# Kernel tuning notes

Hardware: AMD Instinct MI355X
Metric: run time of the kernel (lower is better)

## Reference

```python
import jax, jax.numpy as jnp
import numpy as np

TOKENS, DIM, DIM_OUT, R, ALPHA = 8192, 4096, 4096, 16, 32
SCALE = ALPHA / R  # 2.0


def setup_inputs() -> dict:
    key = jax.random.key(0)
    k1, k2, k3, k4, k5 = jax.random.split(key, 5)
    x = jax.random.normal(k1, (TOKENS, DIM), dtype=jnp.float32)
    A = jax.random.normal(k2, (DIM, R), dtype=jnp.float32)
    B = jax.random.normal(k3, (R, DIM_OUT), dtype=jnp.float32) * 0.02
    W = jax.random.normal(k4, (DIM_OUT, DIM), dtype=jnp.float32) * 0.02  # base Linear weight
    b = jax.random.normal(k5, (DIM_OUT,), dtype=jnp.float32)
    return {"x": x, "A": A, "B": B, "W": W, "b": b}


def reference(x, A, B, W, b):
    # LoRA path: x @ (A @ B) * scale, computed in the efficient low-rank order
    # (mathematically identical to materializing the full-rank weight).
    lora = ((x @ A) @ B) * SCALE              # [tokens, dim_out]
    base = x @ W.T + b                         # wrapped base Linear forward
    return lora + base
```

## Files before the change

kernel.cpp:

```cpp
#include <hip/hip_runtime.h>
#include <hip/hip_bf16.h>
#include <stdint.h>

#define TOKENS   8192
#define DIM      4096
#define DIM_OUT  4096
#define LORA_R   16
#define LORA_SCALE 2.0f

typedef __bf16 bf16_t;
typedef __attribute__((ext_vector_type(8))) __bf16 bfrag;
typedef __attribute__((ext_vector_type(4))) float f32x4;

__device__ __forceinline__ void gload_lds16(const bf16_t* gsrc, bf16_t* ldst) {
    __builtin_amdgcn_global_load_lds(
        (const __attribute__((address_space(1))) uint32_t*)(const void*)gsrc,
        (__attribute__((address_space(3))) uint32_t*)(void*)ldst,
        16, 0, 0);
}

__global__ void cast_x_kernel(const float* __restrict__ x, bf16_t* __restrict__ xb) {
    const int total = TOKENS * DIM / 8;
    for (int i = blockIdx.x * blockDim.x + threadIdx.x; i < total;
         i += gridDim.x * blockDim.x) {
        const float4* p = reinterpret_cast<const float4*>(x + (size_t)i * 8);
        float4 v0 = p[0], v1 = p[1];
        union { bf16_t o[8]; uint4 u; } pk;
        pk.o[0] = (bf16_t)v0.x; pk.o[1] = (bf16_t)v0.y;
        pk.o[2] = (bf16_t)v0.z; pk.o[3] = (bf16_t)v0.w;
        pk.o[4] = (bf16_t)v1.x; pk.o[5] = (bf16_t)v1.y;
        pk.o[6] = (bf16_t)v1.z; pk.o[7] = (bf16_t)v1.w;
        *reinterpret_cast<uint4*>(xb + (size_t)i * 8) = pk.u;
    }
}

__global__ void weff_kernel(const float* __restrict__ W, const float* __restrict__ A,
                            const float* __restrict__ B, bf16_t* __restrict__ Wt) {
    int idx = blockIdx.x * blockDim.x + threadIdx.x;
    int k0 = (idx & 511) << 3;
    int n0 = (idx >> 9) << 2;

    float bn[4][16];
#pragma unroll
    for (int r = 0; r < 16; ++r) {
        float4 bv = *reinterpret_cast<const float4*>(B + (size_t)r * DIM_OUT + n0);
        bn[0][r] = bv.x; bn[1][r] = bv.y; bn[2][r] = bv.z; bn[3][r] = bv.w;
    }
    float ab[4][8];
#pragma unroll
    for (int j = 0; j < 8; ++j) {
        const float4* ap = reinterpret_cast<const float4*>(A + (size_t)(k0 + j) * LORA_R);
        float4 a0 = ap[0], a1 = ap[1], a2 = ap[2], a3 = ap[3];
        float av[16] = {a0.x,a0.y,a0.z,a0.w,a1.x,a1.y,a1.z,a1.w,
                        a2.x,a2.y,a2.z,a2.w,a3.x,a3.y,a3.z,a3.w};
#pragma unroll
        for (int n = 0; n < 4; ++n) {
            float s = 0.f;
#pragma unroll
            for (int r = 0; r < 16; ++r) s += av[r] * bn[n][r];
            ab[n][j] = s;
        }
    }
#pragma unroll
    for (int n = 0; n < 4; ++n) {
        const float4* wp = reinterpret_cast<const float4*>(W + (size_t)(n0 + n) * DIM + k0);
        float4 w0 = wp[0], w1 = wp[1];
        float wv[8] = {w0.x,w0.y,w0.z,w0.w,w1.x,w1.y,w1.z,w1.w};
        union { bf16_t o[8]; uint4 u; } pk;
#pragma unroll
        for (int j = 0; j < 8; ++j) pk.o[j] = (bf16_t)(wv[j] + LORA_SCALE * ab[n][j]);
        *reinterpret_cast<uint4*>(Wt + (size_t)(n0 + n) * DIM + k0) = pk.u;
    }
}

#define BM 256
#define BN 256
#define BK 64
#define MB_BLKS (TOKENS / BM)
#define NB_BLKS (DIM_OUT / BN)
#define NT      (DIM / BK)

#define BAR() do { __builtin_amdgcn_s_barrier(); __builtin_amdgcn_sched_barrier(0); } while (0)
#define SB0() __builtin_amdgcn_sched_barrier(0)
#define VMWAIT_(n) asm volatile("s_waitcnt vmcnt(" #n ")" ::: "memory")
#define VMWAIT(n) VMWAIT_(n)

__global__ __launch_bounds__(512, 2) void gemm_kernel(
    const bf16_t* __restrict__ Xb, const bf16_t* __restrict__ Wt,
    const float* __restrict__ bias, float* __restrict__ C)
{
    __shared__ __align__(16) bf16_t sA[2][BM][BK];
    __shared__ __align__(16) bf16_t sB[2][BN][BK];

    const int nwg = MB_BLKS * NB_BLKS;
    int bid = blockIdx.x;
    int swz = (bid & 7) * (nwg >> 3) + (bid >> 3);
    int bm = swz / NB_BLKS;
    int bn = swz % NB_BLKS;

    const int tid  = threadIdx.x;
    const int lane = tid & 63;
    const int wid  = tid >> 6;
    const int wr   = wid >> 2;
    const int wc   = wid & 3;

    const int srow = tid >> 3;
    const int scol = (tid & 7) * 8;
    const int koff = (((tid & 7) ^ ((tid >> 3) & 7)) * 8);
    const bf16_t* Ag = Xb + (size_t)(bm * BM + srow) * DIM + koff;
    const bf16_t* Bg = Wt + (size_t)(bn * BN + srow) * DIM + koff;

#define STAGE_A(d, kt) do { \
    const bf16_t* s_ = Ag + (size_t)(kt) * BK; \
    bf16_t* d_ = &sA[d][srow][scol]; \
    gload_lds16(s_,                     d_); \
    gload_lds16(s_ + (size_t)64  * DIM, d_ + 64  * BK); \
    gload_lds16(s_ + (size_t)128 * DIM, d_ + 128 * BK); \
    gload_lds16(s_ + (size_t)192 * DIM, d_ + 192 * BK); \
} while (0)

#define STAGE_B(d, kt) do { \
    const bf16_t* s_ = Bg + (size_t)(kt) * BK; \
    bf16_t* d_ = &sB[d][srow][scol]; \
    gload_lds16(s_,                     d_); \
    gload_lds16(s_ + (size_t)64  * DIM, d_ + 64  * BK); \
    gload_lds16(s_ + (size_t)128 * DIM, d_ + 128 * BK); \
    gload_lds16(s_ + (size_t)192 * DIM, d_ + 192 * BK); \
} while (0)

    const int q     = lane & 7;
    const int kslot = lane >> 4;
    const int r15   = lane & 15;
    const int cK0   = ((kslot    ) ^ q) * 8;
    const int cK1   = ((kslot + 4) ^ q) * 8;
    const int arow0 = wr * 128 + r15;
    const int brow0 = wc * 64  + r15;

    f32x4 acc[8][4] = {};
    bfrag aLo[4][2], aHi[4][2], bLo[2][2], bHi[2][2];

#define READ_A4(dst, dd, mb) do { \
    _Pragma("unroll") \
    for (int m_ = 0; m_ < 4; ++m_) { \
        dst[m_][0] = *reinterpret_cast<const bfrag*>(&sA[dd][arow0 + (mb + m_) * 16][cK0]); \
        dst[m_][1] = *reinterpret_cast<const bfrag*>(&sA[dd][arow0 + (mb + m_) * 16][cK1]); \
    } \
} while (0)

#define READ_B2(dst, dd, nb) do { \
    _Pragma("unroll") \
    for (int n_ = 0; n_ < 2; ++n_) { \
        dst[n_][0] = *reinterpret_cast<const bfrag*>(&sB[dd][brow0 + (nb + n_) * 16][cK0]); \
        dst[n_][1] = *reinterpret_cast<const bfrag*>(&sB[dd][brow0 + (nb + n_) * 16][cK1]); \
    } \
} while (0)

#define MFMA_Q(Af, Bf, mb, nb) do { \
    __builtin_amdgcn_s_setprio(1); \
    _Pragma("unroll") \
    for (int m_ = 0; m_ < 4; ++m_) \
    _Pragma("unroll") \
    for (int n_ = 0; n_ < 2; ++n_) \
    _Pragma("unroll") \
    for (int ks_ = 0; ks_ < 2; ++ks_) \
        acc[mb + m_][nb + n_] = __builtin_amdgcn_mfma_f32_16x16x32_bf16( \
            Af[m_][ks_], Bf[n_][ks_], acc[mb + m_][nb + n_], 0, 0, 0); \
    __builtin_amdgcn_s_setprio(0); \
} while (0)

#define TILE(d, ktn, DO_STAGE, DO_NEXT, VM) do { \
     READ_B2(bHi, d, 2); \
             SB0(); MFMA_Q(aLo, bLo, 0, 0); BAR(); \
     READ_A4(aHi, d, 4); if (DO_STAGE) STAGE_B(d, ktn); \
             SB0(); MFMA_Q(aLo, bHi, 0, 2); VMWAIT(VM); BAR(); \
     if (DO_NEXT) READ_A4(aLo, (d) ^ 1, 0); if (DO_STAGE) STAGE_A(d, ktn); \
             SB0(); MFMA_Q(aHi, bHi, 4, 2); BAR(); \
     MFMA_Q(aHi, bLo, 4, 0); \
             if (DO_NEXT) READ_B2(bLo, (d) ^ 1, 0); BAR(); \
} while (0)

    STAGE_A(0, 0); STAGE_B(0, 0);
    STAGE_B(1, 1); STAGE_A(1, 1);
    VMWAIT(8);
    BAR();
    READ_A4(aLo, 0, 0); READ_B2(bLo, 0, 0);

    for (int it = 0; it < NT / 2 - 1; ++it) {
        int kt0 = 2 * it;
        TILE(0, kt0 + 2, true, true, 4);
        TILE(1, kt0 + 3, true, true, 4);
    }
    TILE(0, 0, false, true, 0);
    TILE(1, 0, false, false, 0);

    int row0 = bm * BM + wr * 128 + (lane >> 4) * 4;
    int col0 = bn * BN + wc * 64 + r15;
#pragma unroll
    for (int n = 0; n < 4; ++n) {
        int c = col0 + n * 16;
        float bv = bias[c];
#pragma unroll
        for (int m = 0; m < 8; ++m) {
            int r = row0 + m * 16;
#pragma unroll
            for (int j = 0; j < 4; ++j)
                C[(size_t)(r + j) * DIM_OUT + c] = acc[m][n][j] + bv;
        }
    }
}

extern "C" void kernel_launch(void* const* d_in, const int* in_sizes, int n_in,
                              void* d_out, int out_size, void* d_ws, size_t ws_size,
                              hipStream_t stream) {
    const float* x = (const float*)d_in[0];
    const float* A = (const float*)d_in[1];
    const float* B = (const float*)d_in[2];
    const float* W = (const float*)d_in[3];
    const float* b = (const float*)d_in[4];
    float* out = (float*)d_out;

    bf16_t* xb = (bf16_t*)d_ws;
    bf16_t* Wt = (bf16_t*)((char*)d_ws + (size_t)TOKENS * DIM * 2);

    cast_x_kernel<<<2048, 256, 0, stream>>>(x, xb);
    weff_kernel<<<(DIM_OUT * DIM / 32) / 256, 256, 0, stream>>>(W, A, B, Wt);
    gemm_kernel<<<MB_BLKS * NB_BLKS, 512, 0, stream>>>(xb, Wt, b, out);
}
```

Measured before the change: 329.4 us.

## Restructure GEMM pipeline with half-tile staging and a single A fragment buffer

Reworks the main GEMM loop schedule. Global-to-LDS loads are split into half-tiles and spread across the four MFMA phases of each tile, with one A half staged a tile ahead. A fragments now use a single buffer instead of lo/hi pairs, which lowers register pressure, and explicit lgkmcnt waits plus extra barriers are added before each MFMA group. The cost is more barriers and LDS reads that are no longer prefetched from the next tile, which may expose LDS latency.

```diff
diff --git a/kernel.cpp b/kernel.cpp
--- a/kernel.cpp
+++ b/kernel.cpp
@@ -80,8 +80,9 @@
 #define NB_BLKS (DIM_OUT / BN)
 #define NT      (DIM / BK)
 
-#define BAR() do { __builtin_amdgcn_s_barrier(); __builtin_amdgcn_sched_barrier(0); } while (0)
 #define SB0() __builtin_amdgcn_sched_barrier(0)
+#define BAR() do { SB0(); __builtin_amdgcn_s_barrier(); SB0(); } while (0)
+#define LGKM0() do { asm volatile("s_waitcnt lgkmcnt(0)" ::: "memory"); SB0(); } while (0)
 #define VMWAIT_(n) asm volatile("s_waitcnt vmcnt(" #n ")" ::: "memory")
 #define VMWAIT(n) VMWAIT_(n)
 
@@ -110,22 +111,18 @@
     const bf16_t* Ag = Xb + (size_t)(bm * BM + srow) * DIM + koff;
     const bf16_t* Bg = Wt + (size_t)(bn * BN + srow) * DIM + koff;
 
-#define STAGE_A(d, kt) do { \
-    const bf16_t* s_ = Ag + (size_t)(kt) * BK; \
-    bf16_t* d_ = &sA[d][srow][scol]; \
-    gload_lds16(s_,                     d_); \
-    gload_lds16(s_ + (size_t)64  * DIM, d_ + 64  * BK); \
-    gload_lds16(s_ + (size_t)128 * DIM, d_ + 128 * BK); \
-    gload_lds16(s_ + (size_t)192 * DIM, d_ + 192 * BK); \
-} while (0)
-
-#define STAGE_B(d, kt) do { \
-    const bf16_t* s_ = Bg + (size_t)(kt) * BK; \
-    bf16_t* d_ = &sB[d][srow][scol]; \
-    gload_lds16(s_,                     d_); \
-    gload_lds16(s_ + (size_t)64  * DIM, d_ + 64  * BK); \
-    gload_lds16(s_ + (size_t)128 * DIM, d_ + 128 * BK); \
-    gload_lds16(s_ + (size_t)192 * DIM, d_ + 192 * BK); \
+#define STAGE_A_H(dd, kt, h) do { \
+    const bf16_t* s_ = Ag + (size_t)(kt) * BK + (size_t)((h) * 128) * DIM; \
+    bf16_t* d_ = &sA[dd][(h) * 128 + srow][scol]; \
+    gload_lds16(s_,                    d_); \
+    gload_lds16(s_ + (size_t)64 * DIM, d_ + 64 * BK); \
+} while (0)
+
+#define STAGE_B_H(dd, kt, h) do { \
+    const bf16_t* s_ = Bg + (size_t)(kt) * BK + (size_t)((h) * 128) * DIM; \
+    bf16_t* d_ = &sB[dd][(h) * 128 + srow][scol]; \
+    gload_lds16(s_,                    d_); \
+    gload_lds16(s_ + (size_t)64 * DIM, d_ + 64 * BK); \
 } while (0)
 
     const int q     = lane & 7;
@@ -137,7 +134,7 @@
     const int brow0 = wc * 64  + r15;
 
     f32x4 acc[8][4] = {};
-    bfrag aLo[4][2], aHi[4][2], bLo[2][2], bHi[2][2];
+    bfrag a[4][2], bLo[2][2], bHi[2][2];
 
 #define READ_A4(dst, dd, mb) do { \
     _Pragma("unroll") \
@@ -168,30 +165,31 @@
     __builtin_amdgcn_s_setprio(0); \
 } while (0)
 
-#define TILE(d, ktn, DO_STAGE, DO_NEXT, VM) do { \
+#define TILE(d, kt, S1, S2, VM) do { \
+     READ_A4(a, d, 0); READ_B2(bLo, d, 0); \
+             BAR(); LGKM0(); MFMA_Q(a, bLo, 0, 0); BAR(); \
      READ_B2(bHi, d, 2); \
-             SB0(); MFMA_Q(aLo, bLo, 0, 0); BAR(); \
-     READ_A4(aHi, d, 4); if (DO_STAGE) STAGE_B(d, ktn); \
-             SB0(); MFMA_Q(aLo, bHi, 0, 2); VMWAIT(VM); BAR(); \
-     if (DO_NEXT) READ_A4(aLo, (d) ^ 1, 0); if (DO_STAGE) STAGE_A(d, ktn); \
-             SB0(); MFMA_Q(aHi, bHi, 4, 2); BAR(); \
-     MFMA_Q(aHi, bLo, 4, 0); \
-             if (DO_NEXT) READ_B2(bLo, (d) ^ 1, 0); BAR(); \
-} while (0)
-
-    STAGE_A(0, 0); STAGE_B(0, 0);
-    STAGE_B(1, 1); STAGE_A(1, 1);
-    VMWAIT(8);
+             if (S1) STAGE_A_H((d) ^ 1, (kt) + 1, 1); \
+             BAR(); LGKM0(); MFMA_Q(a, bHi, 0, 2); BAR(); \
+     READ_A4(a, d, 4); \
+             if (S2) STAGE_B_H(d, (kt) + 2, 0); \
+             BAR(); LGKM0(); MFMA_Q(a, bHi, 4, 2); BAR(); \
+     if (S2) { STAGE_B_H(d, (kt) + 2, 1); STAGE_A_H(d, (kt) + 2, 0); } \
+             BAR(); MFMA_Q(a, bLo, 4, 0); VMWAIT(VM); BAR(); \
+} while (0)
+
+    STAGE_A_H(0, 0, 0); STAGE_A_H(0, 0, 1); STAGE_B_H(0, 0, 0); STAGE_B_H(0, 0, 1);
+    STAGE_A_H(1, 1, 0); STAGE_B_H(1, 1, 0); STAGE_B_H(1, 1, 1);
+    VMWAIT(6);
     BAR();
-    READ_A4(aLo, 0, 0); READ_B2(bLo, 0, 0);
 
     for (int it = 0; it < NT / 2 - 1; ++it) {
         int kt0 = 2 * it;
-        TILE(0, kt0 + 2, true, true, 4);
-        TILE(1, kt0 + 3, true, true, 4);
-    }
-    TILE(0, 0, false, true, 0);
-    TILE(1, 0, false, false, 0);
+        TILE(0, kt0,     true, true, 6);
+        TILE(1, kt0 + 1, true, true, 6);
+    }
+    TILE(0, 62, true,  false, 0);
+    TILE(1, 63, false, false, 0);
 
     int row0 = bm * BM + wr * 128 + (lane >> 4) * 4;
     int col0 = bn * BN + wc * 64 + r15;
```

Result: slower. 346.4 us (+5.2%).

## Switch GEMM inner loop from 16x16x32 to 32x32x16 bf16 MFMA tiles

Applied to the files above, without the earlier changes.

Replaces the 16x16x32 MFMA fragments with 32x32x16 MFMA instructions. The per-wave accumulator layout, LDS fragment reads with their XOR-swizzled k-slots, and the epilogue store indexing are all rewritten to match the 32x32 output layout. The larger MFMA cuts the number of instructions and LDS fragment loads per unit of work. The trade-off is different register pressure and a different LDS bank access pattern.

```diff
diff --git a/kernel.cpp b/kernel.cpp
--- a/kernel.cpp
+++ b/kernel.cpp
@@ -10,7 +10,7 @@
 
 typedef __bf16 bf16_t;
 typedef __attribute__((ext_vector_type(8))) __bf16 bfrag;
-typedef __attribute__((ext_vector_type(4))) float f32x4;
+typedef __attribute__((ext_vector_type(16))) float f32x16;
 
 __device__ __forceinline__ void gload_lds16(const bf16_t* gsrc, bf16_t* ldst) {
     __builtin_amdgcn_global_load_lds(
@@ -80,8 +80,8 @@
 #define NB_BLKS (DIM_OUT / BN)
 #define NT      (DIM / BK)
 
-#define BAR() do { __builtin_amdgcn_s_barrier(); __builtin_amdgcn_sched_barrier(0); } while (0)
 #define SB0() __builtin_amdgcn_sched_barrier(0)
+#define BAR() do { __builtin_amdgcn_s_barrier(); SB0(); } while (0)
 #define VMWAIT_(n) asm volatile("s_waitcnt vmcnt(" #n ")" ::: "memory")
 #define VMWAIT(n) VMWAIT_(n)
 
@@ -110,80 +110,79 @@
     const bf16_t* Ag = Xb + (size_t)(bm * BM + srow) * DIM + koff;
     const bf16_t* Bg = Wt + (size_t)(bn * BN + srow) * DIM + koff;
 
-#define STAGE_A(d, kt) do { \
+#define STAGE_A(dd, kt) do { \
     const bf16_t* s_ = Ag + (size_t)(kt) * BK; \
-    bf16_t* d_ = &sA[d][srow][scol]; \
+    bf16_t* d_ = &sA[dd][srow][scol]; \
     gload_lds16(s_,                     d_); \
     gload_lds16(s_ + (size_t)64  * DIM, d_ + 64  * BK); \
     gload_lds16(s_ + (size_t)128 * DIM, d_ + 128 * BK); \
     gload_lds16(s_ + (size_t)192 * DIM, d_ + 192 * BK); \
 } while (0)
 
-#define STAGE_B(d, kt) do { \
+#define STAGE_B(dd, kt) do { \
     const bf16_t* s_ = Bg + (size_t)(kt) * BK; \
-    bf16_t* d_ = &sB[d][srow][scol]; \
+    bf16_t* d_ = &sB[dd][srow][scol]; \
     gload_lds16(s_,                     d_); \
     gload_lds16(s_ + (size_t)64  * DIM, d_ + 64  * BK); \
     gload_lds16(s_ + (size_t)128 * DIM, d_ + 128 * BK); \
     gload_lds16(s_ + (size_t)192 * DIM, d_ + 192 * BK); \
 } while (0)
 
-    const int q     = lane & 7;
-    const int kslot = lane >> 4;
-    const int r15   = lane & 15;
-    const int cK0   = ((kslot    ) ^ q) * 8;
-    const int cK1   = ((kslot + 4) ^ q) * 8;
-    const int arow0 = wr * 128 + r15;
-    const int brow0 = wc * 64  + r15;
-
-    f32x4 acc[8][4] = {};
-    bfrag aLo[4][2], aHi[4][2], bLo[2][2], bHi[2][2];
-
-#define READ_A4(dst, dd, mb) do { \
-    _Pragma("unroll") \
-    for (int m_ = 0; m_ < 4; ++m_) { \
-        dst[m_][0] = *reinterpret_cast<const bfrag*>(&sA[dd][arow0 + (mb + m_) * 16][cK0]); \
-        dst[m_][1] = *reinterpret_cast<const bfrag*>(&sA[dd][arow0 + (mb + m_) * 16][cK1]); \
-    } \
-} while (0)
-
-#define READ_B2(dst, dd, nb) do { \
-    _Pragma("unroll") \
-    for (int n_ = 0; n_ < 2; ++n_) { \
-        dst[n_][0] = *reinterpret_cast<const bfrag*>(&sB[dd][brow0 + (nb + n_) * 16][cK0]); \
-        dst[n_][1] = *reinterpret_cast<const bfrag*>(&sB[dd][brow0 + (nb + n_) * 16][cK1]); \
-    } \
-} while (0)
-
-#define MFMA_Q(Af, Bf, mb, nb) do { \
+    const int q   = lane & 7;
+    const int kgl = lane >> 5;
+    const int r31 = lane & 31;
+    int cS[4];
+#pragma unroll
+    for (int s = 0; s < 4; ++s) cS[s] = ((2 * s + kgl) ^ q) * 8;
+    const int arow0 = wr * 128 + r31;
+    const int brow0 = wc * 64  + r31;
+
+    f32x16 acc[4][2] = {};
+    bfrag aLo[2][4], aHi[2][4], bLo[4], bHi[4];
+
+#define READ_A2(dst, dd, mb0) do { \
+    _Pragma("unroll") \
+    for (int m_ = 0; m_ < 2; ++m_) \
+    _Pragma("unroll") \
+    for (int s_ = 0; s_ < 4; ++s_) \
+        dst[m_][s_] = *reinterpret_cast<const bfrag*>( \
+            &sA[dd][arow0 + (mb0 + m_) * 32][cS[s_]]); \
+} while (0)
+
+#define READ_B1(dst, dd, nb) do { \
+    _Pragma("unroll") \
+    for (int s_ = 0; s_ < 4; ++s_) \
+        dst[s_] = *reinterpret_cast<const bfrag*>( \
+            &sB[dd][brow0 + (nb) * 32][cS[s_]]); \
+} while (0)
+
+#define MFMA_Q(Af, Bf, mb0, nb) do { \
     __builtin_amdgcn_s_setprio(1); \
     _Pragma("unroll") \
-    for (int m_ = 0; m_ < 4; ++m_) \
-    _Pragma("unroll") \
-    for (int n_ = 0; n_ < 2; ++n_) \
-    _Pragma("unroll") \
-    for (int ks_ = 0; ks_ < 2; ++ks_) \
-        acc[mb + m_][nb + n_] = __builtin_amdgcn_mfma_f32_16x16x32_bf16( \
-            Af[m_][ks_], Bf[n_][ks_], acc[mb + m_][nb + n_], 0, 0, 0); \
+    for (int s_ = 0; s_ < 4; ++s_) \
+    _Pragma("unroll") \
+    for (int m_ = 0; m_ < 2; ++m_) \
+        acc[mb0 + m_][nb] = __builtin_amdgcn_mfma_f32_32x32x16_bf16( \
+            Af[m_][s_], Bf[s_], acc[mb0 + m_][nb], 0, 0, 0); \
     __builtin_amdgcn_s_setprio(0); \
 } while (0)
 
-#define TILE(d, ktn, DO_STAGE, DO_NEXT, VM) do { \
-     READ_B2(bHi, d, 2); \
+#define TILE(d, ktn, S, NEXT, VM) do { \
+     READ_B1(bHi, d, 1); \
              SB0(); MFMA_Q(aLo, bLo, 0, 0); BAR(); \
-     READ_A4(aHi, d, 4); if (DO_STAGE) STAGE_B(d, ktn); \
-             SB0(); MFMA_Q(aLo, bHi, 0, 2); VMWAIT(VM); BAR(); \
-     if (DO_NEXT) READ_A4(aLo, (d) ^ 1, 0); if (DO_STAGE) STAGE_A(d, ktn); \
-             SB0(); MFMA_Q(aHi, bHi, 4, 2); BAR(); \
-     MFMA_Q(aHi, bLo, 4, 0); \
-             if (DO_NEXT) READ_B2(bLo, (d) ^ 1, 0); BAR(); \
+     READ_A2(aHi, d, 2); if (S) STAGE_B(d, ktn); \
+             SB0(); MFMA_Q(aLo, bHi, 0, 1); VMWAIT(VM); BAR(); \
+     if (NEXT) READ_A2(aLo, (d) ^ 1, 0); if (S) STAGE_A(d, ktn); \
+             SB0(); MFMA_Q(aHi, bHi, 2, 1); BAR(); \
+     MFMA_Q(aHi, bLo, 2, 0); \
+             if (NEXT) READ_B1(bLo, (d) ^ 1, 0); BAR(); \
 } while (0)
 
     STAGE_A(0, 0); STAGE_B(0, 0);
     STAGE_B(1, 1); STAGE_A(1, 1);
     VMWAIT(8);
     BAR();
-    READ_A4(aLo, 0, 0); READ_B2(bLo, 0, 0);
+    READ_A2(aLo, 0, 0); READ_B1(bLo, 0, 0);
 
     for (int it = 0; it < NT / 2 - 1; ++it) {
         int kt0 = 2 * it;
@@ -193,18 +192,20 @@
     TILE(0, 0, false, true, 0);
     TILE(1, 0, false, false, 0);
 
-    int row0 = bm * BM + wr * 128 + (lane >> 4) * 4;
-    int col0 = bn * BN + wc * 64 + r15;
-#pragma unroll
-    for (int n = 0; n < 4; ++n) {
-        int c = col0 + n * 16;
+    const int colbase = bn * BN + wc * 64 + r31;
+    const int rowbase = bm * BM + wr * 128 + 4 * kgl;
+#pragma unroll
+    for (int n = 0; n < 2; ++n) {
+        int c = colbase + n * 32;
         float bv = bias[c];
 #pragma unroll
-        for (int m = 0; m < 8; ++m) {
-            int r = row0 + m * 16;
-#pragma unroll
-            for (int j = 0; j < 4; ++j)
-                C[(size_t)(r + j) * DIM_OUT + c] = acc[m][n][j] + bv;
+        for (int m = 0; m < 4; ++m) {
+            int rb = rowbase + m * 32;
+#pragma unroll
+            for (int reg = 0; reg < 16; ++reg) {
+                int r = rb + (reg & 3) + 8 * (reg >> 2);
+                C[(size_t)r * DIM_OUT + c] = acc[m][n][reg] + bv;
+            }
         }
     }
 }
```

Result: slower. 346.8 us (+5.3%).

## Fuse prep kernels into one launch and rotate GEMM tile pipeline phases

Applied to the files above, without the earlier changes.

Merges the x-cast and effective-weight kernels into a single launch, split by block index, which removes one kernel launch and lets both prep tasks share the GPU at once. Restructures the GEMM main loop into a 3-barrier tile: the next tile's B-high fragment read and first MFMA quadrant move to the end of the previous tile, with a prologue that issues them before the loop. This cuts one barrier per K-tile and overlaps LDS reads with MFMA work. It also raises register pressure, because both bLo and bHi for the next tile are live at the same time.

```diff
diff --git a/kernel.cpp b/kernel.cpp
--- a/kernel.cpp
+++ b/kernel.cpp
@@ -19,57 +19,59 @@
         16, 0, 0);
 }
 
-__global__ void cast_x_kernel(const float* __restrict__ x, bf16_t* __restrict__ xb) {
-    const int total = TOKENS * DIM / 8;
-    for (int i = blockIdx.x * blockDim.x + threadIdx.x; i < total;
-         i += gridDim.x * blockDim.x) {
-        const float4* p = reinterpret_cast<const float4*>(x + (size_t)i * 8);
-        float4 v0 = p[0], v1 = p[1];
-        union { bf16_t o[8]; uint4 u; } pk;
-        pk.o[0] = (bf16_t)v0.x; pk.o[1] = (bf16_t)v0.y;
-        pk.o[2] = (bf16_t)v0.z; pk.o[3] = (bf16_t)v0.w;
-        pk.o[4] = (bf16_t)v1.x; pk.o[5] = (bf16_t)v1.y;
-        pk.o[6] = (bf16_t)v1.z; pk.o[7] = (bf16_t)v1.w;
-        *reinterpret_cast<uint4*>(xb + (size_t)i * 8) = pk.u;
-    }
-}
-
-__global__ void weff_kernel(const float* __restrict__ W, const float* __restrict__ A,
+#define CAST_BLOCKS 2048
+__global__ void prep_kernel(const float* __restrict__ x, bf16_t* __restrict__ xb,
+                            const float* __restrict__ W, const float* __restrict__ A,
                             const float* __restrict__ B, bf16_t* __restrict__ Wt) {
-    int idx = blockIdx.x * blockDim.x + threadIdx.x;
-    int k0 = (idx & 511) << 3;
-    int n0 = (idx >> 9) << 2;
-
-    float bn[4][16];
-#pragma unroll
-    for (int r = 0; r < 16; ++r) {
-        float4 bv = *reinterpret_cast<const float4*>(B + (size_t)r * DIM_OUT + n0);
-        bn[0][r] = bv.x; bn[1][r] = bv.y; bn[2][r] = bv.z; bn[3][r] = bv.w;
-    }
-    float ab[4][8];
-#pragma unroll
-    for (int j = 0; j < 8; ++j) {
-        const float4* ap = reinterpret_cast<const float4*>(A + (size_t)(k0 + j) * LORA_R);
-        float4 a0 = ap[0], a1 = ap[1], a2 = ap[2], a3 = ap[3];
-        float av[16] = {a0.x,a0.y,a0.z,a0.w,a1.x,a1.y,a1.z,a1.w,
-                        a2.x,a2.y,a2.z,a2.w,a3.x,a3.y,a3.z,a3.w};
+    if (blockIdx.x < CAST_BLOCKS) {
+        const int total = TOKENS * DIM / 8;
+        for (int i = blockIdx.x * blockDim.x + threadIdx.x; i < total;
+             i += CAST_BLOCKS * 256) {
+            const float4* p = reinterpret_cast<const float4*>(x + (size_t)i * 8);
+            float4 v0 = p[0], v1 = p[1];
+            union { bf16_t o[8]; uint4 u; } pk;
+            pk.o[0] = (bf16_t)v0.x; pk.o[1] = (bf16_t)v0.y;
+            pk.o[2] = (bf16_t)v0.z; pk.o[3] = (bf16_t)v0.w;
+            pk.o[4] = (bf16_t)v1.x; pk.o[5] = (bf16_t)v1.y;
+            pk.o[6] = (bf16_t)v1.z; pk.o[7] = (bf16_t)v1.w;
+            *reinterpret_cast<uint4*>(xb + (size_t)i * 8) = pk.u;
+        }
+    } else {
+        int idx = (blockIdx.x - CAST_BLOCKS) * blockDim.x + threadIdx.x;
+        int k0 = (idx & 511) << 3;
+        int n0 = (idx >> 9) << 2;
+
+        float bn[4][16];
+#pragma unroll
+        for (int r = 0; r < 16; ++r) {
+            float4 bv = *reinterpret_cast<const float4*>(B + (size_t)r * DIM_OUT + n0);
+            bn[0][r] = bv.x; bn[1][r] = bv.y; bn[2][r] = bv.z; bn[3][r] = bv.w;
+        }
+        float ab[4][8];
+#pragma unroll
+        for (int j = 0; j < 8; ++j) {
+            const float4* ap = reinterpret_cast<const float4*>(A + (size_t)(k0 + j) * LORA_R);
+            float4 a0 = ap[0], a1 = ap[1], a2 = ap[2], a3 = ap[3];
+            float av[16] = {a0.x,a0.y,a0.z,a0.w,a1.x,a1.y,a1.z,a1.w,
+                            a2.x,a2.y,a2.z,a2.w,a3.x,a3.y,a3.z,a3.w};
+#pragma unroll
+            for (int n = 0; n < 4; ++n) {
+                float s = 0.f;
+#pragma unroll
+                for (int r = 0; r < 16; ++r) s += av[r] * bn[n][r];
+                ab[n][j] = s;
+            }
+        }
 #pragma unroll
         for (int n = 0; n < 4; ++n) {
-            float s = 0.f;
-#pragma unroll
-            for (int r = 0; r < 16; ++r) s += av[r] * bn[n][r];
-            ab[n][j] = s;
-        }
-    }
-#pragma unroll
-    for (int n = 0; n < 4; ++n) {
-        const float4* wp = reinterpret_cast<const float4*>(W + (size_t)(n0 + n) * DIM + k0);
-        float4 w0 = wp[0], w1 = wp[1];
-        float wv[8] = {w0.x,w0.y,w0.z,w0.w,w1.x,w1.y,w1.z,w1.w};
-        union { bf16_t o[8]; uint4 u; } pk;
-#pragma unroll
-        for (int j = 0; j < 8; ++j) pk.o[j] = (bf16_t)(wv[j] + LORA_SCALE * ab[n][j]);
-        *reinterpret_cast<uint4*>(Wt + (size_t)(n0 + n) * DIM + k0) = pk.u;
+            const float4* wp = reinterpret_cast<const float4*>(W + (size_t)(n0 + n) * DIM + k0);
+            float4 w0 = wp[0], w1 = wp[1];
+            float wv[8] = {w0.x,w0.y,w0.z,w0.w,w1.x,w1.y,w1.z,w1.w};
+            union { bf16_t o[8]; uint4 u; } pk;
+#pragma unroll
+            for (int j = 0; j < 8; ++j) pk.o[j] = (bf16_t)(wv[j] + LORA_SCALE * ab[n][j]);
+            *reinterpret_cast<uint4*>(Wt + (size_t)(n0 + n) * DIM + k0) = pk.u;
+        }
     }
 }
 
@@ -80,8 +82,8 @@
 #define NB_BLKS (DIM_OUT / BN)
 #define NT      (DIM / BK)
 
-#define BAR() do { __builtin_amdgcn_s_barrier(); __builtin_amdgcn_sched_barrier(0); } while (0)
 #define SB0() __builtin_amdgcn_sched_barrier(0)
+#define BAR() do { __builtin_amdgcn_s_barrier(); SB0(); } while (0)
 #define VMWAIT_(n) asm volatile("s_waitcnt vmcnt(" #n ")" ::: "memory")
 #define VMWAIT(n) VMWAIT_(n)
 
@@ -110,18 +112,18 @@
     const bf16_t* Ag = Xb + (size_t)(bm * BM + srow) * DIM + koff;
     const bf16_t* Bg = Wt + (size_t)(bn * BN + srow) * DIM + koff;
 
-#define STAGE_A(d, kt) do { \
+#define STAGE_A(dd, kt) do { \
     const bf16_t* s_ = Ag + (size_t)(kt) * BK; \
-    bf16_t* d_ = &sA[d][srow][scol]; \
+    bf16_t* d_ = &sA[dd][srow][scol]; \
     gload_lds16(s_,                     d_); \
     gload_lds16(s_ + (size_t)64  * DIM, d_ + 64  * BK); \
     gload_lds16(s_ + (size_t)128 * DIM, d_ + 128 * BK); \
     gload_lds16(s_ + (size_t)192 * DIM, d_ + 192 * BK); \
 } while (0)
 
-#define STAGE_B(d, kt) do { \
+#define STAGE_B(dd, kt) do { \
     const bf16_t* s_ = Bg + (size_t)(kt) * BK; \
-    bf16_t* d_ = &sB[d][srow][scol]; \
+    bf16_t* d_ = &sB[dd][srow][scol]; \
     gload_lds16(s_,                     d_); \
     gload_lds16(s_ + (size_t)64  * DIM, d_ + 64  * BK); \
     gload_lds16(s_ + (size_t)128 * DIM, d_ + 128 * BK); \
@@ -168,30 +170,35 @@
     __builtin_amdgcn_s_setprio(0); \
 } while (0)
 
-#define TILE(d, ktn, DO_STAGE, DO_NEXT, VM) do { \
-     READ_B2(bHi, d, 2); \
-             SB0(); MFMA_Q(aLo, bLo, 0, 0); BAR(); \
-     READ_A4(aHi, d, 4); if (DO_STAGE) STAGE_B(d, ktn); \
+#define TILE3(d, ktn, S, NEXTQ, VM) do { \
+     READ_A4(aHi, d, 4); if (S) STAGE_B(d, ktn); \
              SB0(); MFMA_Q(aLo, bHi, 0, 2); VMWAIT(VM); BAR(); \
-     if (DO_NEXT) READ_A4(aLo, (d) ^ 1, 0); if (DO_STAGE) STAGE_A(d, ktn); \
+     if (NEXTQ) READ_A4(aLo, (d) ^ 1, 0); if (S) STAGE_A(d, ktn); \
              SB0(); MFMA_Q(aHi, bHi, 4, 2); BAR(); \
      MFMA_Q(aHi, bLo, 4, 0); \
-             if (DO_NEXT) READ_B2(bLo, (d) ^ 1, 0); BAR(); \
+             if (NEXTQ) { \
+                 READ_B2(bLo, (d) ^ 1, 0); READ_B2(bHi, (d) ^ 1, 2); \
+                 MFMA_Q(aLo, bLo, 0, 0); \
+             } \
+             BAR(); \
 } while (0)
 
     STAGE_A(0, 0); STAGE_B(0, 0);
     STAGE_B(1, 1); STAGE_A(1, 1);
     VMWAIT(8);
     BAR();
-    READ_A4(aLo, 0, 0); READ_B2(bLo, 0, 0);
+    READ_A4(aLo, 0, 0); READ_B2(bLo, 0, 0); READ_B2(bHi, 0, 2);
+    SB0();
+    MFMA_Q(aLo, bLo, 0, 0);
+    BAR();
 
     for (int it = 0; it < NT / 2 - 1; ++it) {
         int kt0 = 2 * it;
-        TILE(0, kt0 + 2, true, true, 4);
-        TILE(1, kt0 + 3, true, true, 4);
+        TILE3(0, kt0 + 2, true, true, 4);
+        TILE3(1, kt0 + 3, true, true, 4);
     }
-    TILE(0, 0, false, true, 0);
-    TILE(1, 0, false, false, 0);
+    TILE3(0, 0, false, true, 0);
+    TILE3(1, 0, false, false, 0);
 
     int row0 = bm * BM + wr * 128 + (lane >> 4) * 4;
     int col0 = bn * BN + wc * 64 + r15;
@@ -222,7 +229,6 @@
     bf16_t* xb = (bf16_t*)d_ws;
     bf16_t* Wt = (bf16_t*)((char*)d_ws + (size_t)TOKENS * DIM * 2);
 
-    cast_x_kernel<<<2048, 256, 0, stream>>>(x, xb);
-    weff_kernel<<<(DIM_OUT * DIM / 32) / 256, 256, 0, stream>>>(W, A, B, Wt);
+    prep_kernel<<<CAST_BLOCKS + 2048, 256, 0, stream>>>(x, xb, W, A, B, Wt);
     gemm_kernel<<<MB_BLKS * NB_BLKS, 512, 0, stream>>>(xb, Wt, b, out);
 }
```

After: 325.4 us. About the same (-1.2%).
